# Optimization experiments

Hardware: AMD Instinct MI355X
Metric: run time of the kernel (lower is better)

Reference implementation:

```python
import jax, jax.numpy as jnp
import numpy as np

N = 8192
H = 512
TAU = 0.8
LAM = 0.5
EPS = 1e-8


def setup_inputs() -> dict:
    key = jax.random.key(0)
    k1, k2, k3, k4, k5 = jax.random.split(key, 5)
    xavier_std = 1.414 * np.sqrt(2.0 / (H + H))  # xavier_normal_ with gain=1.414
    return {
        "z_mp": jax.random.normal(k1, (N, H), dtype=jnp.float32),
        "z_sc": jax.random.normal(k2, (N, H), dtype=jnp.float32),
        "pos": jax.random.randint(k3, (N, N), 0, 2, dtype=jnp.int32),
        "W1": (jax.random.normal(k4, (H, H), dtype=jnp.float32) * xavier_std),
        "b1": jnp.zeros((H,), dtype=jnp.float32),
        "W2": (jax.random.normal(k5, (H, H), dtype=jnp.float32) * xavier_std),
        "b2": jnp.zeros((H,), dtype=jnp.float32),
    }


def _proj(z, W1, b1, W2, b2):
    # nn.Linear applies x @ W.T + b
    h = jax.nn.elu(z @ W1.T + b1)
    return h @ W2.T + b2


def _sim(z1, z2, tau):
    # exp(cosine_similarity / tau), computed as in the original:
    # dot(z1, z2.T) / (|z1| |z2|.T) / tau
    n1 = jnp.linalg.norm(z1, axis=-1, keepdims=True)  # [N,1]
    n2 = jnp.linalg.norm(z2, axis=-1, keepdims=True)  # [N,1]
    dot = z1 @ z2.T                                   # [N,N]
    return jnp.exp(dot / (n1 * n2.T) / tau)


def reference(z_mp, z_sc, pos, W1, b1, W2, b2):
    pos_f = pos.astype(jnp.float32)
    zp_mp = _proj(z_mp, W1, b1, W2, b2)
    zp_sc = _proj(z_sc, W1, b1, W2, b2)

    m_mp2sc = _sim(zp_mp, zp_sc, TAU)   # [N,N]
    m_sc2mp = m_mp2sc.T                 # [N,N]

    # row-normalize, masked log-mean (mp -> sc)
    s_mp = m_mp2sc / (jnp.sum(m_mp2sc, axis=1, keepdims=True) + EPS)
    lori_mp = -jnp.mean(jnp.log(jnp.sum(s_mp * pos_f, axis=-1)))

    # row-normalize, masked log-mean (sc -> mp)
    s_sc = m_sc2mp / (jnp.sum(m_sc2mp, axis=1, keepdims=True) + EPS)
    lori_sc = -jnp.mean(jnp.log(jnp.sum(s_sc * pos_f, axis=-1)))

    return LAM * lori_mp + (1.0 - LAM) * lori_sc
```

## Files before the change

kernel.cpp:

```cpp
#include <hip/hip_runtime.h>
#include <stdint.h>


#define NN 8192
#define HH 512
#define TAUF 0.8f
#define EPSF 1e-8f
#define NW (NN / 32)

typedef __attribute__((ext_vector_type(8))) short short8;
typedef __attribute__((ext_vector_type(4))) float f32x4;
typedef __attribute__((ext_vector_type(4))) int i32x4;
typedef __attribute__((ext_vector_type(8))) int i32x8;
typedef __attribute__((ext_vector_type(4))) unsigned short u16x4;
typedef unsigned short u16;
typedef unsigned int u32;
typedef uint8_t u8;

typedef __attribute__((address_space(1))) void GV;
typedef __attribute__((address_space(3))) void LV;

__device__ __forceinline__ void g2l16(const void* g, void* l) {
  __builtin_amdgcn_global_load_lds((const GV*)g, (LV*)l, 16, 0, 0);
}

__device__ __forceinline__ u16 f2bf(float x) {
  u32 u = __builtin_bit_cast(u32, x);
  u = (u + 0x7fffu + ((u >> 16) & 1u)) >> 16;
  return (u16)u;
}

__device__ __forceinline__ u32 f2fp8(float x) {
  u32 u = __builtin_bit_cast(u32, x);
  u32 s = (u >> 31) << 7;
  float a = fabsf(x);
  if (a >= 0.015625f) {
    u32 b = __builtin_bit_cast(u32, a);
    b += 0x7FFFFu + ((b >> 20) & 1u);
    u32 e = (b >> 23) - 127u + 7u;
    u32 m = (b >> 20) & 7u;
    return s | (e << 3) | m;
  } else {
    int m = (int)rintf(a * 512.0f);
    return s | (u32)m;
  }
}

__device__ __forceinline__ void cast8(const float* __restrict__ in, u16* __restrict__ out, int i) {
  f32x4 a = *(const f32x4*)(in + i);
  f32x4 b = *(const f32x4*)(in + i + 4);
  u16 o[8];
  o[0] = f2bf(a.x); o[1] = f2bf(a.y); o[2] = f2bf(a.z); o[3] = f2bf(a.w);
  o[4] = f2bf(b.x); o[5] = f2bf(b.y); o[6] = f2bf(b.z); o[7] = f2bf(b.w);
  i32x4 v;
  v.x = (int)(o[0] | ((u32)o[1] << 16)); v.y = (int)(o[2] | ((u32)o[3] << 16));
  v.z = (int)(o[4] | ((u32)o[5] << 16)); v.w = (int)(o[6] | ((u32)o[7] << 16));
  *(i32x4*)(out + i) = v;
}

__global__ __launch_bounds__(256)
void prep_kernel(const int* __restrict__ pos, u32* __restrict__ P,
                 const float* __restrict__ z_mp, u16* __restrict__ zbA,
                 const float* __restrict__ z_sc, u16* __restrict__ zbB,
                 const float* __restrict__ W1, u16* __restrict__ W1b,
                 const float* __restrict__ W2, u16* __restrict__ W2b) {
  int b = blockIdx.x, tid = threadIdx.x;
  if (b < 8192) {
    int gid = b * 256 + tid;
    const int* src = pos + (size_t)gid * 32;
    u32 w = 0;
#pragma unroll
    for (int c = 0; c < 8; ++c) {
      i32x4 p = *(const i32x4*)(src + c * 4);
      w |= ((u32)p.x & 1u) << (c * 4);
      w |= ((u32)p.y & 1u) << (c * 4 + 1);
      w |= ((u32)p.z & 1u) << (c * 4 + 2);
      w |= ((u32)p.w & 1u) << (c * 4 + 3);
    }
    P[gid] = w;
  } else if (b < 10240) {
    cast8(z_mp, zbA, ((b - 8192) * 256 + tid) * 8);
  } else if (b < 12288) {
    cast8(z_sc, zbB, ((b - 10240) * 256 + tid) * 8);
  } else if (b < 12416) {
    cast8(W1, W1b, ((b - 12288) * 256 + tid) * 8);
  } else {
    cast8(W2, W2b, ((b - 12416) * 256 + tid) * 8);
  }
}

template <int EPI>
__global__ __launch_bounds__(256)
void gemm_proj(const u16* __restrict__ A1, const u16* __restrict__ A2,
               const u16* __restrict__ W, const float* __restrict__ bias,
               void* __restrict__ out1, void* __restrict__ out2) {
  __shared__ __align__(16) u16 As[128 * 32];
  __shared__ __align__(16) u16 Bs[128 * 32];
  const int tid = threadIdx.x;
  const int lane = tid & 63, w = tid >> 6;
  const int lo = lane & 15, quad = lane >> 4;
  const int wy = w >> 1, wx = w & 1;
  const u16* A; char* Out; int m0;
  if (blockIdx.y < 64) { A = A1; Out = (char*)out1; m0 = blockIdx.y * 128; }
  else                 { A = A2; Out = (char*)out2; m0 = (blockIdx.y - 64) * 128; }
  const int n0 = blockIdx.x * 128;
  const int srow = w * 16 + (lane >> 2);
  const int skel = (lane & 3) * 8;
  char* AsB = (char*)As; char* BsB = (char*)Bs;
  f32x4 acc[4][4] = {};

  for (int k0 = 0; k0 < HH; k0 += 32) {
    const u16* ga = A + (size_t)(m0 + srow) * HH + k0 + skel;
    const u16* gb = W + (size_t)(n0 + srow) * HH + k0 + skel;
    g2l16(ga, AsB + w * 1024);
    g2l16(ga + (size_t)64 * HH, AsB + w * 1024 + 4096);
    g2l16(gb, BsB + w * 1024);
    g2l16(gb + (size_t)64 * HH, BsB + w * 1024 + 4096);
    asm volatile("s_waitcnt vmcnt(0)" ::: "memory");
    __syncthreads();
    short8 aF[4], bF[4];
#pragma unroll
    for (int mi = 0; mi < 4; ++mi)
      aF[mi] = *(const short8*)(AsB + (wy * 64 + mi * 16 + lo) * 64 + quad * 16);
#pragma unroll
    for (int ni = 0; ni < 4; ++ni)
      bF[ni] = *(const short8*)(BsB + (wx * 64 + ni * 16 + lo) * 64 + quad * 16);
#pragma unroll
    for (int mi = 0; mi < 4; ++mi)
#pragma unroll
      for (int ni = 0; ni < 4; ++ni)
        acc[mi][ni] = __builtin_amdgcn_mfma_f32_16x16x32_bf16(aF[mi], bF[ni], acc[mi][ni], 0, 0, 0);
    __syncthreads();
  }
#pragma unroll
  for (int mi = 0; mi < 4; ++mi) {
    int rl = wy * 64 + mi * 16 + quad * 4;
#pragma unroll
    for (int ni = 0; ni < 4; ++ni) {
      int cl = wx * 64 + ni * 16 + lo;
      float bv = bias[n0 + cl];
#pragma unroll
      for (int r = 0; r < 4; ++r) {
        float v = acc[mi][ni][r] + bv;
        size_t idx = (size_t)(m0 + rl + r) * HH + (n0 + cl);
        if (EPI == 0) {
          if (v < 0.f) v = __expf(v) - 1.f;
          ((u16*)Out)[idx] = f2bf(v);
        } else {
          ((float*)Out)[idx] = v;
        }
      }
    }
  }
}

__global__ void norm_kernel(const float* __restrict__ zpA, u8* __restrict__ znA,
                            const float* __restrict__ zpB, u8* __restrict__ znB) {
  const int row = blockIdx.x & (NN - 1);
  const bool isA = blockIdx.x < NN;
  const float* src = (isA ? zpA : zpB) + (size_t)row * HH;
  u8* dst = (isA ? znA : znB) + (size_t)row * HH;
  const float scale = isA ? (1.0f / TAUF) : 1.0f;
  const int t = threadIdx.x;
  f32x4 v = *(const f32x4*)(src + t * 4);
  float ss = v.x * v.x + v.y * v.y + v.z * v.z + v.w * v.w;
#pragma unroll
  for (int d = 1; d < 64; d <<= 1) ss += __shfl_xor(ss, d, 64);
  __shared__ float red[2];
  if ((t & 63) == 0) red[t >> 6] = ss;
  __syncthreads();
  float inv = scale * rsqrtf(red[0] + red[1]);
  u32 o = f2fp8(v.x * inv) | (f2fp8(v.y * inv) << 8) |
          (f2fp8(v.z * inv) << 16) | (f2fp8(v.w * inv) << 24);
  *(u32*)(dst + t * 4) = o;
}

__global__ __launch_bounds__(256)
void sim_kernel(const u8* __restrict__ Az, const u8* __restrict__ Bz,
                const u32* __restrict__ Pbits,
                float* __restrict__ rowpart, float* __restrict__ posrowpart,
                float* __restrict__ colpart, float* __restrict__ poscolpart) {
  __shared__ __align__(16) u8 As[128 * 128];
  __shared__ __align__(16) u8 Bs[128 * 128];
  __shared__ u32 PBi[128 * 4];
  __shared__ u32 PBj[128 * 4];
  const int tid = threadIdx.x;
  const int lane = tid & 63, w = tid >> 6;
  const int lo = lane & 15, quad = lane >> 4;
  const int wy = w >> 1, wx = w & 1;

  const int bid = blockIdx.x + (int)gridDim.x * blockIdx.y;
  const int xcd = bid & 7, s = bid >> 3;
  const int by = xcd * 8 + (s >> 6);
  const int bx = s & 63;
  const int i0 = by * 128, j0 = bx * 128;

  const int il = tid >> 1, w2 = (tid & 1) * 2;
  const u32* PiSrc = Pbits + (size_t)(i0 + il) * NW + (j0 >> 5) + w2;
  const u32* PjSrc = Pbits + (size_t)(j0 + il) * NW + (i0 >> 5) + w2;
  u32 pa0 = PiSrc[0], pa1 = PiSrc[1], pb0 = PjSrc[0], pb1 = PjSrc[1];

  const int srow = lane >> 3;
  const int schunk = ((lane & 7) ^ srow) * 16;
  char* AsB = (char*)As; char* BsB = (char*)Bs;
  f32x4 acc[4][4] = {};

  for (int k0 = 0; k0 < HH; k0 += 128) {
    const u8* ga = Az + (size_t)(i0 + w * 32 + srow) * HH + k0 + schunk;
    const u8* gb = Bz + (size_t)(j0 + w * 32 + srow) * HH + k0 + schunk;
#pragma unroll
    for (int t = 0; t < 4; ++t) {
      g2l16(ga + (size_t)(t * 8) * HH, AsB + w * 4096 + t * 1024);
      g2l16(gb + (size_t)(t * 8) * HH, BsB + w * 4096 + t * 1024);
    }
    asm volatile("s_waitcnt vmcnt(0)" ::: "memory");
    __syncthreads();
    i32x8 aF[4], bF[4];
#pragma unroll
    for (int mi = 0; mi < 4; ++mi) {
      int ar = wy * 64 + mi * 16 + lo;
      int sw = ar & 7;
      i32x4 p0 = *(const i32x4*)(AsB + ar * 128 + ((2 * quad) ^ sw) * 16);
      i32x4 p1 = *(const i32x4*)(AsB + ar * 128 + ((2 * quad + 1) ^ sw) * 16);
      aF[mi] = __builtin_shufflevector(p0, p1, 0, 1, 2, 3, 4, 5, 6, 7);
    }
#pragma unroll
    for (int ni = 0; ni < 4; ++ni) {
      int br = wx * 64 + ni * 16 + lo;
      int sw = br & 7;
      i32x4 p0 = *(const i32x4*)(BsB + br * 128 + ((2 * quad) ^ sw) * 16);
      i32x4 p1 = *(const i32x4*)(BsB + br * 128 + ((2 * quad + 1) ^ sw) * 16);
      bF[ni] = __builtin_shufflevector(p0, p1, 0, 1, 2, 3, 4, 5, 6, 7);
    }
#pragma unroll
    for (int mi = 0; mi < 4; ++mi)
#pragma unroll
      for (int ni = 0; ni < 4; ++ni)
        acc[mi][ni] = __builtin_amdgcn_mfma_scale_f32_16x16x128_f8f6f4(
            aF[mi], bF[ni], acc[mi][ni], 0, 0, 0, 127, 0, 127);
    __syncthreads();
  }

  PBi[il * 4 + w2] = pa0; PBi[il * 4 + w2 + 1] = pa1;
  PBj[il * 4 + w2] = pb0; PBj[il * 4 + w2 + 1] = pb1;

#pragma unroll
  for (int mi = 0; mi < 4; ++mi)
#pragma unroll
    for (int ni = 0; ni < 4; ++ni)
#pragma unroll
      for (int r = 0; r < 4; ++r)
        acc[mi][ni][r] = __expf(acc[mi][ni][r]);

  __syncthreads();

  const int rowb = wy * 64 + quad * 4;
  const int colb = wx * 64 + lo;

#pragma unroll
  for (int mi = 0; mi < 4; ++mi) {
    int rl = rowb + mi * 16;
    float rs[4], pr[4];
#pragma unroll
    for (int r = 0; r < 4; ++r) {
      u32 W0 = PBi[(rl + r) * 4 + wx * 2];
      u32 W1 = PBi[(rl + r) * 4 + wx * 2 + 1];
      float e0 = acc[mi][0][r], e1 = acc[mi][1][r];
      float e2 = acc[mi][2][r], e3 = acc[mi][3][r];
      rs[r] = (e0 + e1) + (e2 + e3);
      pr[r] = (((W0 >> lo) & 1u) ? e0 : 0.f) + (((W0 >> (16 + lo)) & 1u) ? e1 : 0.f) +
              (((W1 >> lo) & 1u) ? e2 : 0.f) + (((W1 >> (16 + lo)) & 1u) ? e3 : 0.f);
    }
#pragma unroll
    for (int d = 1; d < 16; d <<= 1) {
#pragma unroll
      for (int r = 0; r < 4; ++r) {
        rs[r] += __shfl_xor(rs[r], d, 64);
        pr[r] += __shfl_xor(pr[r], d, 64);
      }
    }
    if (lo == 0) {
      float* rp = rowpart + (size_t)(bx * 2 + wx) * NN;
      float* pp = posrowpart + (size_t)(bx * 2 + wx) * NN;
#pragma unroll
      for (int r = 0; r < 4; ++r) {
        rp[i0 + rl + r] = rs[r];
        pp[i0 + rl + r] = pr[r];
      }
    }
  }

#pragma unroll
  for (int ni = 0; ni < 4; ++ni) {
    int cl = colb + ni * 16;
    u32 W0 = PBj[cl * 4 + wy * 2];
    u32 W1 = PBj[cl * 4 + wy * 2 + 1];
    float cs = 0.f, pc = 0.f;
#pragma unroll
    for (int mi = 0; mi < 4; ++mi) {
      u32 W = (mi < 2) ? W0 : W1;
      int sh = (mi & 1) * 16 + quad * 4;
#pragma unroll
      for (int r = 0; r < 4; ++r) {
        float e = acc[mi][ni][r];
        cs += e;
        pc += ((W >> (sh + r)) & 1u) ? e : 0.f;
      }
    }
    cs += __shfl_xor(cs, 16, 64); cs += __shfl_xor(cs, 32, 64);
    pc += __shfl_xor(pc, 16, 64); pc += __shfl_xor(pc, 32, 64);
    if (quad == 0) {
      colpart[(size_t)(by * 2 + wy) * NN + j0 + cl] = cs;
      poscolpart[(size_t)(by * 2 + wy) * NN + j0 + cl] = pc;
    }
  }
}

__global__ __launch_bounds__(256)
void reduce1_kernel(const float* __restrict__ rowpart, const float* __restrict__ posrowpart,
                    const float* __restrict__ colpart, const float* __restrict__ poscolpart,
                    float* __restrict__ red) {
  int t = threadIdx.x;
  int i = blockIdx.x * 128 + (t >> 1);
  int half = t & 1;
  float rs = 0.f, pr = 0.f, cs = 0.f, pc = 0.f;
  for (int s = half * 64; s < half * 64 + 64; ++s) {
    rs += rowpart[(size_t)s * NN + i];
    pr += posrowpart[(size_t)s * NN + i];
    cs += colpart[(size_t)s * NN + i];
    pc += poscolpart[(size_t)s * NN + i];
  }
  rs += __shfl_xor(rs, 1, 64); pr += __shfl_xor(pr, 1, 64);
  cs += __shfl_xor(cs, 1, 64); pc += __shfl_xor(pc, 1, 64);
  float term = (half == 0) ? (__logf(pr / (rs + EPSF)) + __logf(pc / (cs + EPSF))) : 0.f;
#pragma unroll
  for (int d = 2; d < 64; d <<= 1) term += __shfl_xor(term, d, 64);
  __shared__ float rsh[4];
  if ((t & 63) == 0) rsh[t >> 6] = term;
  __syncthreads();
  if (t == 0) red[blockIdx.x] = rsh[0] + rsh[1] + rsh[2] + rsh[3];
}

__global__ void reduce2_kernel(const float* __restrict__ red, float* __restrict__ out) {
  float s = red[threadIdx.x];
#pragma unroll
  for (int d = 1; d < 64; d <<= 1) s += __shfl_xor(s, d, 64);
  if (threadIdx.x == 0) out[0] = -0.5f * s / (float)NN;
}

extern "C" void kernel_launch(void* const* d_in, const int* in_sizes, int n_in,
                              void* d_out, int out_size, void* d_ws, size_t ws_size,
                              hipStream_t stream) {
  const float* z_mp = (const float*)d_in[0];
  const float* z_sc = (const float*)d_in[1];
  const int* pos = (const int*)d_in[2];
  const float* W1 = (const float*)d_in[3];
  const float* b1 = (const float*)d_in[4];
  const float* W2 = (const float*)d_in[5];
  const float* b2 = (const float*)d_in[6];
  float* out = (float*)d_out;

  char* ws = (char*)d_ws;
  u32* Pbits = (u32*)(ws);
  u16* zbA = (u16*)(ws + 8388608);
  u16* zbB = (u16*)(ws + 16777216);
  u16* W1b = (u16*)(ws + 25165824);
  u16* W2b = (u16*)(ws + 25690112);
  u16* hA  = (u16*)(ws + 26214400);
  u16* hB  = (u16*)(ws + 34603008);
  float* zpA = (float*)(ws + 42991616);
  float* zpB = (float*)(ws + 59768832);
  u8* znA = (u8*)zbA;
  u8* znB = (u8*)zbB;
  float* rowpart    = (float*)(ws + 26214400);
  float* posrowpart = (float*)(ws + 30408704);
  float* colpart    = (float*)(ws + 34603008);
  float* poscolpart = (float*)(ws + 38797312);
  float* red64 = (float*)(ws + 76546048);

  prep_kernel<<<12544, 256, 0, stream>>>(pos, Pbits, z_mp, zbA, z_sc, zbB, W1, W1b, W2, W2b);

  dim3 gp(4, 128);
  gemm_proj<0><<<gp, 256, 0, stream>>>(zbA, zbB, W1b, b1, hA, hB);
  gemm_proj<1><<<gp, 256, 0, stream>>>(hA, hB, W2b, b2, zpA, zpB);

  norm_kernel<<<2 * NN, 128, 0, stream>>>(zpA, znA, zpB, znB);

  dim3 gs(64, 64);
  sim_kernel<<<gs, 256, 0, stream>>>(znA, znB, Pbits, rowpart, posrowpart, colpart, poscolpart);
  reduce1_kernel<<<64, 256, 0, stream>>>(rowpart, posrowpart, colpart, poscolpart, red64);
  reduce2_kernel<<<1, 64, 0, stream>>>(red64, out);
}
```

Baseline: 534.3 us.

## Store fp8 embeddings in MFMA fragment layout and load directly from global

The norm kernel now writes the fp8 normalized embeddings in a pre-tiled layout that matches the MFMA operand fragments (16-row groups, 32-byte chunks per lane). The sim kernel drops its LDS staging of A/B tiles and their barriers, loading fragments straight from global memory into registers with a one-step register double buffer across the K loop. This removes LDS traffic and __syncthreads, but each wave now fetches its fragments from global or L2 independently, so there is less on-chip sharing between waves and more vector registers are used.

```diff
diff --git a/kernel.cpp b/kernel.cpp
--- a/kernel.cpp
+++ b/kernel.cpp
@@ -159,7 +159,7 @@
   const int row = blockIdx.x & (NN - 1);
   const bool isA = blockIdx.x < NN;
   const float* src = (isA ? zpA : zpB) + (size_t)row * HH;
-  u8* dst = (isA ? znA : znB) + (size_t)row * HH;
+  u8* dst = (isA ? znA : znB);
   const float scale = isA ? (1.0f / TAUF) : 1.0f;
   const int t = threadIdx.x;
   f32x4 v = *(const f32x4*)(src + t * 4);
@@ -172,7 +172,13 @@
   float inv = scale * rsqrtf(red[0] + red[1]);
   u32 o = f2fp8(v.x * inv) | (f2fp8(v.y * inv) << 8) |
           (f2fp8(v.z * inv) << 16) | (f2fp8(v.w * inv) << 24);
-  *(u32*)(dst + t * 4) = o;
+  *(u32*)(dst + (size_t)(row >> 4) * 8192 + (t >> 3) * 512 + (row & 15) * 32 + (t & 7) * 4) = o;
+}
+
+__device__ __forceinline__ i32x8 ld_frag(const u8* p) {
+  i32x4 p0 = *(const i32x4*)p;
+  i32x4 p1 = *(const i32x4*)(p + 16);
+  return __builtin_shufflevector(p0, p1, 0, 1, 2, 3, 4, 5, 6, 7);
 }
 
 __global__ __launch_bounds__(256)
@@ -180,8 +186,6 @@
                 const u32* __restrict__ Pbits,
                 float* __restrict__ rowpart, float* __restrict__ posrowpart,
                 float* __restrict__ colpart, float* __restrict__ poscolpart) {
-  __shared__ __align__(16) u8 As[128 * 128];
-  __shared__ __align__(16) u8 Bs[128 * 128];
   __shared__ u32 PBi[128 * 4];
   __shared__ u32 PBj[128 * 4];
   const int tid = threadIdx.x;
@@ -200,45 +204,36 @@
   const u32* PjSrc = Pbits + (size_t)(j0 + il) * NW + (i0 >> 5) + w2;
   u32 pa0 = PiSrc[0], pa1 = PiSrc[1], pb0 = PjSrc[0], pb1 = PjSrc[1];
 
-  const int srow = lane >> 3;
-  const int schunk = ((lane & 7) ^ srow) * 16;
-  char* AsB = (char*)As; char* BsB = (char*)Bs;
+  const int lof = quad * 512 + lo * 32;
+  const u8* Ab = Az + (size_t)((i0 >> 4) + wy * 4) * 8192 + lof;
+  const u8* Bb = Bz + (size_t)((j0 >> 4) + wx * 4) * 8192 + lof;
+
   f32x4 acc[4][4] = {};
-
-  for (int k0 = 0; k0 < HH; k0 += 128) {
-    const u8* ga = Az + (size_t)(i0 + w * 32 + srow) * HH + k0 + schunk;
-    const u8* gb = Bz + (size_t)(j0 + w * 32 + srow) * HH + k0 + schunk;
-#pragma unroll
-    for (int t = 0; t < 4; ++t) {
-      g2l16(ga + (size_t)(t * 8) * HH, AsB + w * 4096 + t * 1024);
-      g2l16(gb + (size_t)(t * 8) * HH, BsB + w * 4096 + t * 1024);
-    }
-    asm volatile("s_waitcnt vmcnt(0)" ::: "memory");
-    __syncthreads();
-    i32x8 aF[4], bF[4];
-#pragma unroll
-    for (int mi = 0; mi < 4; ++mi) {
-      int ar = wy * 64 + mi * 16 + lo;
-      int sw = ar & 7;
-      i32x4 p0 = *(const i32x4*)(AsB + ar * 128 + ((2 * quad) ^ sw) * 16);
-      i32x4 p1 = *(const i32x4*)(AsB + ar * 128 + ((2 * quad + 1) ^ sw) * 16);
-      aF[mi] = __builtin_shufflevector(p0, p1, 0, 1, 2, 3, 4, 5, 6, 7);
-    }
-#pragma unroll
-    for (int ni = 0; ni < 4; ++ni) {
-      int br = wx * 64 + ni * 16 + lo;
-      int sw = br & 7;
-      i32x4 p0 = *(const i32x4*)(BsB + br * 128 + ((2 * quad) ^ sw) * 16);
-      i32x4 p1 = *(const i32x4*)(BsB + br * 128 + ((2 * quad + 1) ^ sw) * 16);
-      bF[ni] = __builtin_shufflevector(p0, p1, 0, 1, 2, 3, 4, 5, 6, 7);
+  i32x8 aC[4], bC[4], aN[4], bN[4];
+#pragma unroll
+  for (int t = 0; t < 4; ++t) {
+    aC[t] = ld_frag(Ab + (size_t)t * 8192);
+    bC[t] = ld_frag(Bb + (size_t)t * 8192);
+  }
+#pragma unroll
+  for (int kq = 0; kq < 4; ++kq) {
+    if (kq < 3) {
+#pragma unroll
+      for (int t = 0; t < 4; ++t) {
+        aN[t] = ld_frag(Ab + (size_t)t * 8192 + (kq + 1) * 2048);
+        bN[t] = ld_frag(Bb + (size_t)t * 8192 + (kq + 1) * 2048);
+      }
     }
 #pragma unroll
     for (int mi = 0; mi < 4; ++mi)
 #pragma unroll
       for (int ni = 0; ni < 4; ++ni)
         acc[mi][ni] = __builtin_amdgcn_mfma_scale_f32_16x16x128_f8f6f4(
-            aF[mi], bF[ni], acc[mi][ni], 0, 0, 0, 127, 0, 127);
-    __syncthreads();
+            aC[mi], bC[ni], acc[mi][ni], 0, 0, 0, 127, 0, 127);
+    if (kq < 3) {
+#pragma unroll
+      for (int t = 0; t < 4; ++t) { aC[t] = aN[t]; bC[t] = bN[t]; }
+    }
   }
 
   PBi[il * 4 + w2] = pa0; PBi[il * 4 + w2 + 1] = pa1;
```

Measured after the change: 567.6 us. +6.2%, slower.
